# Kernel tuning notes

Measured on AMD Instinct MI355X. Metric: run time of the kernel, lower is better.

## Reference

```python
import jax, jax.numpy as jnp
import numpy as np

HID = 1024
HEADS = 16
HEAD_DIM = HID // HEADS


def setup_inputs() -> dict:
    key = jax.random.key(0)
    ks = jax.random.split(key, 11)
    s = 1.0 / np.sqrt(HID)
    return {
        "query": jax.random.normal(ks[0], (4, 2048, HID), jnp.float32),
        "key": jax.random.normal(ks[1], (4, 2048, HID), jnp.float32),
        "value": jax.random.normal(ks[2], (4, 2048, HID), jnp.float32),
        "wq": jax.random.normal(ks[3], (HID, HID), jnp.float32) * s,
        "bq": jnp.zeros((HID,), jnp.float32),
        "wk": jax.random.normal(ks[4], (HID, HID), jnp.float32) * s,
        "bk": jnp.zeros((HID,), jnp.float32),
        "wv": jax.random.normal(ks[5], (HID, HID), jnp.float32) * s,
        "bv": jnp.zeros((HID,), jnp.float32),
        "wo": jax.random.normal(ks[6], (HID, HID), jnp.float32) * s,
        "bo": jnp.zeros((HID,), jnp.float32),
    }


def reference(query, key, value, wq, bq, wk, bk, wv, bv, wo, bo):
    b, s, _ = query.shape
    scale = jnp.sqrt(jnp.asarray(HEAD_DIM, query.dtype))
    # linear projections; weights stored as [in, out]
    Q = (query @ wq + bq).reshape(b, s, HEADS, HEAD_DIM).transpose(0, 2, 1, 3)
    K = (key @ wk + bk).reshape(b, s, HEADS, HEAD_DIM).transpose(0, 2, 1, 3)
    V = (value @ wv + bv).reshape(b, s, HEADS, HEAD_DIM).transpose(0, 2, 1, 3)
    energy = jnp.einsum('bhqd,bhkd->bhqk', Q, K) / scale  # [B,H,S,S]
    attention = jax.nn.softmax(energy, axis=-1)  # dropout p=0 -> identity
    x = jnp.einsum('bhqk,bhkd->bhqd', attention, V)
    x = x.transpose(0, 2, 1, 3).reshape(b, s, HID)
    return x @ wo + bo
```

## Files before the change

kernel.cpp:

```cpp
#include <hip/hip_runtime.h>
#include <hip/hip_bf16.h>

#define B_   4
#define S_   2048
#define HID_ 1024
#define H_   16
#define D_   64
#define M_   (B_ * S_)

typedef __attribute__((ext_vector_type(8))) short bf16x8;
typedef __attribute__((ext_vector_type(4))) float f32x4;

#define GAS __attribute__((address_space(1)))
#define LAS __attribute__((address_space(3)))

__device__ __forceinline__ unsigned short f2bf(float f) {
    union { float f; unsigned int u; } x; x.f = f;
    unsigned int u = x.u;
    return (unsigned short)((u + 0x7fffu + ((u >> 16) & 1u)) >> 16);
}

__global__ __launch_bounds__(256)
void cast_bf16(const float* __restrict__ in, unsigned short* __restrict__ out) {
    const int i = blockIdx.x * 256 + threadIdx.x;
    const f32x4 a = ((const f32x4*)in)[i * 2];
    const f32x4 b = ((const f32x4*)in)[i * 2 + 1];
    bf16x8 v;
#pragma unroll
    for (int j = 0; j < 4; j++) { v[j] = (short)f2bf(a[j]); v[4 + j] = (short)f2bf(b[j]); }
    ((bf16x8*)out)[i] = v;
}

__global__ void transpose_cast(const float* __restrict__ w0, const float* __restrict__ w1,
                               const float* __restrict__ w2, const float* __restrict__ w3,
                               unsigned short* __restrict__ o0, unsigned short* __restrict__ o1,
                               unsigned short* __restrict__ o2, unsigned short* __restrict__ o3) {
    __shared__ float t[32][33];
    const float* w = (blockIdx.z == 0) ? w0 : (blockIdx.z == 1) ? w1 : (blockIdx.z == 2) ? w2 : w3;
    unsigned short* o = (blockIdx.z == 0) ? o0 : (blockIdx.z == 1) ? o1 : (blockIdx.z == 2) ? o2 : o3;
    const int tx = threadIdx.x, ty = threadIdx.y;
    const int bx = blockIdx.x * 32, by = blockIdx.y * 32;
#pragma unroll
    for (int i = 0; i < 4; i++)
        t[ty + i * 8][tx] = w[(size_t)(by + ty + i * 8) * HID_ + bx + tx];
    __syncthreads();
#pragma unroll
    for (int i = 0; i < 4; i++)
        o[(size_t)(bx + ty + i * 8) * HID_ + by + tx] = f2bf(t[tx][ty + i * 8]);
}

template <int MODE>
__global__ __launch_bounds__(256)
void gemm_k(const unsigned short* __restrict__ A, const unsigned short* __restrict__ Bt,
            const float* __restrict__ bias, void* __restrict__ outp, float oscale) {
    constexpr int BK = 32;
    __shared__ unsigned short As[128 * BK];
    __shared__ unsigned short Bs[128 * BK];

    const int tid  = threadIdx.x;
    const int lane = tid & 63;
    const int wave = tid >> 6;
    const int quad = lane >> 4;
    const int col  = lane & 15;
    const int wm   = (wave & 1) * 64;
    const int wn   = (wave >> 1) * 64;
    const int m0   = blockIdx.x * 128;
    const int n0   = blockIdx.y * 128;

    const int grow = wave * 16 + (lane >> 2);
    const int gcol = (lane & 3) * 8;
    const unsigned short* agp = A  + (size_t)(m0 + grow) * HID_ + gcol;
    const unsigned short* bgp = Bt + (size_t)(n0 + grow) * HID_ + gcol;
    unsigned short* asb = &As[wave * 512];
    unsigned short* bsb = &Bs[wave * 512];

    f32x4 zero; zero[0] = 0.f; zero[1] = 0.f; zero[2] = 0.f; zero[3] = 0.f;
    f32x4 acc[4][4];
#pragma unroll
    for (int mi = 0; mi < 4; mi++)
#pragma unroll
        for (int ni = 0; ni < 4; ni++) acc[mi][ni] = zero;

    for (int kt = 0; kt < HID_; kt += BK) {
        __builtin_amdgcn_global_load_lds((const GAS unsigned int*)(agp + kt),
                                         (LAS unsigned int*)asb, 16, 0, 0);
        __builtin_amdgcn_global_load_lds((const GAS unsigned int*)(agp + kt + (size_t)64 * HID_),
                                         (LAS unsigned int*)(asb + 2048), 16, 0, 0);
        __builtin_amdgcn_global_load_lds((const GAS unsigned int*)(bgp + kt),
                                         (LAS unsigned int*)bsb, 16, 0, 0);
        __builtin_amdgcn_global_load_lds((const GAS unsigned int*)(bgp + kt + (size_t)64 * HID_),
                                         (LAS unsigned int*)(bsb + 2048), 16, 0, 0);
        __syncthreads();

        bf16x8 af[4], bfr[4];
#pragma unroll
        for (int i = 0; i < 4; i++) af[i]  = *(const bf16x8*)&As[(wm + i * 16 + col) * BK + quad * 8];
#pragma unroll
        for (int i = 0; i < 4; i++) bfr[i] = *(const bf16x8*)&Bs[(wn + i * 16 + col) * BK + quad * 8];
#pragma unroll
        for (int mi = 0; mi < 4; mi++)
#pragma unroll
            for (int ni = 0; ni < 4; ni++)
                acc[mi][ni] = __builtin_amdgcn_mfma_f32_16x16x32_bf16(af[mi], bfr[ni], acc[mi][ni], 0, 0, 0);
        __syncthreads();
    }

#pragma unroll
    for (int ni = 0; ni < 4; ni++) {
        const int gn = n0 + wn + ni * 16 + col;
        const float bv = bias[gn];
#pragma unroll
        for (int mi = 0; mi < 4; mi++) {
#pragma unroll
            for (int i = 0; i < 4; i++) {
                const int gm = m0 + wm + mi * 16 + quad * 4 + i;
                const float v = (acc[mi][ni][i] + bv) * oscale;
                if constexpr (MODE == 2) {
                    ((float*)outp)[(size_t)gm * HID_ + gn] = v;
                } else if constexpr (MODE == 0) {
                    const int b = gm >> 11, s = gm & (S_ - 1), h = gn >> 6, d = gn & 63;
                    ((unsigned short*)outp)[(((size_t)b * H_ + h) * S_ + s) * D_ + d] = f2bf(v);
                } else {
                    const int b = gm >> 11, s = gm & (S_ - 1), h = gn >> 6, d = gn & 63;
                    ((unsigned short*)outp)[(((size_t)b * H_ + h) * D_ + d) * S_ + s] = f2bf(v);
                }
            }
        }
    }
}

__global__ __launch_bounds__(256)
void attn_k(const unsigned short* __restrict__ Qp, const unsigned short* __restrict__ Kp,
            const unsigned short* __restrict__ Vt, unsigned short* __restrict__ Xc) {
    constexpr int LK = 72;
    __shared__ unsigned short Ks[64 * LK];
    __shared__ unsigned short Vs[64 * LK];
    __shared__ unsigned short Pb[4][16 * LK];

    const int tid  = threadIdx.x;
    const int lane = tid & 63;
    const int wave = tid >> 6;
    const int quad = lane >> 4;
    const int col  = lane & 15;
    const int bh   = blockIdx.y;
    const int q0   = blockIdx.x * 64 + wave * 16;

    const unsigned short* Qb = Qp + (size_t)bh * S_ * D_;
    const unsigned short* Kb = Kp + (size_t)bh * S_ * D_;
    const unsigned short* Vb = Vt + (size_t)bh * D_ * S_;

    const bf16x8 qf0 = *(const bf16x8*)&Qb[(q0 + col) * D_ + quad * 8];
    const bf16x8 qf1 = *(const bf16x8*)&Qb[(q0 + col) * D_ + 32 + quad * 8];

    const int srow = tid >> 3;
    const int sseg = (tid & 7) * 8;

    f32x4 zero; zero[0] = 0.f; zero[1] = 0.f; zero[2] = 0.f; zero[3] = 0.f;
    f32x4 o[4];
#pragma unroll
    for (int t = 0; t < 4; t++) o[t] = zero;
    float lpart = 0.f;
    unsigned short* pb = &Pb[wave][0];

    for (int c0 = 0; c0 < S_; c0 += 64) {
        {
            const unsigned short* kg = Kb + (size_t)c0 * D_;
#pragma unroll
            for (int p = 0; p < 2; p++) {
                const int row = p * 32 + srow;
                *(bf16x8*)&Ks[row * LK + sseg] = *(const bf16x8*)&kg[row * D_ + sseg];
                *(bf16x8*)&Vs[row * LK + sseg] = *(const bf16x8*)&Vb[(size_t)row * S_ + c0 + sseg];
            }
        }
        __syncthreads();

        f32x4 e[4];
#pragma unroll
        for (int kt = 0; kt < 4; kt++) {
            const bf16x8 ka = *(const bf16x8*)&Ks[(kt * 16 + col) * LK + quad * 8];
            const bf16x8 kb = *(const bf16x8*)&Ks[(kt * 16 + col) * LK + 32 + quad * 8];
            e[kt] = __builtin_amdgcn_mfma_f32_16x16x32_bf16(ka, qf0, zero, 0, 0, 0);
            e[kt] = __builtin_amdgcn_mfma_f32_16x16x32_bf16(kb, qf1, e[kt], 0, 0, 0);
        }

#pragma unroll
        for (int kt = 0; kt < 4; kt++) {
            float p0 = __builtin_amdgcn_exp2f(e[kt][0]);
            float p1 = __builtin_amdgcn_exp2f(e[kt][1]);
            float p2 = __builtin_amdgcn_exp2f(e[kt][2]);
            float p3 = __builtin_amdgcn_exp2f(e[kt][3]);
            lpart += (p0 + p1) + (p2 + p3);
            const unsigned int u0 = __builtin_bit_cast(unsigned int, p0) + 0x8000u;
            const unsigned int u1 = __builtin_bit_cast(unsigned int, p1) + 0x8000u;
            const unsigned int u2 = __builtin_bit_cast(unsigned int, p2) + 0x8000u;
            const unsigned int u3 = __builtin_bit_cast(unsigned int, p3) + 0x8000u;
            uint2 w;
            w.x = __builtin_amdgcn_perm(u1, u0, 0x07060302u);
            w.y = __builtin_amdgcn_perm(u3, u2, 0x07060302u);
            *(uint2*)&pb[col * LK + kt * 16 + quad * 4] = w;
        }

#pragma unroll
        for (int ch = 0; ch < 2; ch++) {
            const bf16x8 pf = *(const bf16x8*)&pb[col * LK + ch * 32 + quad * 8];
#pragma unroll
            for (int t = 0; t < 4; t++) {
                const bf16x8 vf = *(const bf16x8*)&Vs[(t * 16 + col) * LK + ch * 32 + quad * 8];
                o[t] = __builtin_amdgcn_mfma_f32_16x16x32_bf16(vf, pf, o[t], 0, 0, 0);
            }
        }
        __syncthreads();
    }

    float l = lpart;
    l += __shfl_xor(l, 16);
    l += __shfl_xor(l, 32);
    const float inv = 1.f / l;

    const int b = bh >> 4, h = bh & 15;
    const int s = q0 + col;
    unsigned short* xp = &Xc[((size_t)(b * S_ + s)) * HID_ + h * D_];
#pragma unroll
    for (int t = 0; t < 4; t++) {
#pragma unroll
        for (int ii = 0; ii < 2; ii++) {
            const float v0 = o[t][ii * 2] * inv;
            const float v1 = o[t][ii * 2 + 1] * inv;
            const unsigned int wv_ = (unsigned int)f2bf(v0) | ((unsigned int)f2bf(v1) << 16);
            *(unsigned int*)&xp[t * 16 + quad * 4 + ii * 2] = wv_;
        }
    }
}

extern "C" void kernel_launch(void* const* d_in, const int* in_sizes, int n_in,
                              void* d_out, int out_size, void* d_ws, size_t ws_size,
                              hipStream_t stream) {
    (void)in_sizes; (void)n_in; (void)out_size; (void)ws_size;
    const float* query = (const float*)d_in[0];
    const float* key   = (const float*)d_in[1];
    const float* value = (const float*)d_in[2];
    const float* wq    = (const float*)d_in[3];
    const float* bq    = (const float*)d_in[4];
    const float* wk    = (const float*)d_in[5];
    const float* bk    = (const float*)d_in[6];
    const float* wv    = (const float*)d_in[7];
    const float* bv    = (const float*)d_in[8];
    const float* wo    = (const float*)d_in[9];
    const float* bo    = (const float*)d_in[10];
    float* out = (float*)d_out;

    unsigned short* ws  = (unsigned short*)d_ws;
    const size_t WSZ = (size_t)HID_ * HID_;
    const size_t TSZ = (size_t)M_ * HID_;
    unsigned short* wqT = ws;
    unsigned short* wkT = wqT + WSZ;
    unsigned short* wvT = wkT + WSZ;
    unsigned short* woT = wvT + WSZ;
    unsigned short* Qp  = woT + WSZ;
    unsigned short* Kp  = Qp + TSZ;
    unsigned short* Vt  = Kp + TSZ;
    unsigned short* Xc  = Vt + TSZ;
    unsigned short* Xb  = Xc + TSZ;

    const float cvt = 0.125f * 1.44269504f;

    transpose_cast<<<dim3(32, 32, 4), dim3(32, 8), 0, stream>>>(wq, wk, wv, wo, wqT, wkT, wvT, woT);

    const dim3 gg(M_ / 128, HID_ / 128);
    const int cg = (M_ * HID_ / 8) / 256;

    cast_bf16<<<cg, 256, 0, stream>>>(query, Xb);
    gemm_k<0><<<gg, 256, 0, stream>>>(Xb, wqT, bq, Qp, cvt);
    cast_bf16<<<cg, 256, 0, stream>>>(key, Xb);
    gemm_k<0><<<gg, 256, 0, stream>>>(Xb, wkT, bk, Kp, 1.f);
    cast_bf16<<<cg, 256, 0, stream>>>(value, Xb);
    gemm_k<1><<<gg, 256, 0, stream>>>(Xb, wvT, bv, Vt, 1.f);

    attn_k<<<dim3(S_ / 64, B_ * H_), 256, 0, stream>>>(Qp, Kp, Vt, Xc);

    gemm_k<2><<<gg, 256, 0, stream>>>(Xc, woT, bo, out, 1.f);
}
```

Measured before the change: 412.5 us.

## Use 32x32 MFMA in attention and stage GEMM epilogue through LDS

The attention kernel moves from 16x16x32 to 32x32x16 bf16 MFMA with 32 queries per wave and 128 queries per block, which halves the grid and increases reuse of each K/V tile loaded into LDS. The projection GEMM epilogues for Q/K and V now pack bf16 results into a shared buffer and write 16-byte vectorized stores to the head-major and transposed layouts, replacing scattered 2-byte stores. For MODE 0 the MFMA operand order is swapped so each lane holds contiguous output columns. This costs extra shared memory, extra barriers and higher register pressure from the f32x16 accumulators.

```diff
diff --git a/kernel.cpp b/kernel.cpp
--- a/kernel.cpp
+++ b/kernel.cpp
@@ -8,8 +8,9 @@
 #define D_   64
 #define M_   (B_ * S_)
 
-typedef __attribute__((ext_vector_type(8))) short bf16x8;
-typedef __attribute__((ext_vector_type(4))) float f32x4;
+typedef __attribute__((ext_vector_type(8)))  short bf16x8;
+typedef __attribute__((ext_vector_type(4)))  float f32x4;
+typedef __attribute__((ext_vector_type(16))) float f32x16;
 
 #define GAS __attribute__((address_space(1)))
 #define LAS __attribute__((address_space(3)))
@@ -54,8 +55,9 @@
 void gemm_k(const unsigned short* __restrict__ A, const unsigned short* __restrict__ Bt,
             const float* __restrict__ bias, void* __restrict__ outp, float oscale) {
     constexpr int BK = 32;
-    __shared__ unsigned short As[128 * BK];
-    __shared__ unsigned short Bs[128 * BK];
+    __shared__ unsigned short smem[8704];
+    unsigned short* As = smem;
+    unsigned short* Bs = smem + 4096;
 
     const int tid  = threadIdx.x;
     const int lane = tid & 63;
@@ -100,31 +102,80 @@
 #pragma unroll
         for (int mi = 0; mi < 4; mi++)
 #pragma unroll
-            for (int ni = 0; ni < 4; ni++)
-                acc[mi][ni] = __builtin_amdgcn_mfma_f32_16x16x32_bf16(af[mi], bfr[ni], acc[mi][ni], 0, 0, 0);
+            for (int ni = 0; ni < 4; ni++) {
+                if constexpr (MODE == 0)
+                    acc[mi][ni] = __builtin_amdgcn_mfma_f32_16x16x32_bf16(bfr[ni], af[mi], acc[mi][ni], 0, 0, 0);
+                else
+                    acc[mi][ni] = __builtin_amdgcn_mfma_f32_16x16x32_bf16(af[mi], bfr[ni], acc[mi][ni], 0, 0, 0);
+            }
         __syncthreads();
     }
 
-#pragma unroll
-    for (int ni = 0; ni < 4; ni++) {
-        const int gn = n0 + wn + ni * 16 + col;
-        const float bv = bias[gn];
-#pragma unroll
-        for (int mi = 0; mi < 4; mi++) {
-#pragma unroll
-            for (int i = 0; i < 4; i++) {
-                const int gm = m0 + wm + mi * 16 + quad * 4 + i;
-                const float v = (acc[mi][ni][i] + bv) * oscale;
-                if constexpr (MODE == 2) {
-                    ((float*)outp)[(size_t)gm * HID_ + gn] = v;
-                } else if constexpr (MODE == 0) {
-                    const int b = gm >> 11, s = gm & (S_ - 1), h = gn >> 6, d = gn & 63;
-                    ((unsigned short*)outp)[(((size_t)b * H_ + h) * S_ + s) * D_ + d] = f2bf(v);
+    if constexpr (MODE == 2) {
+#pragma unroll
+        for (int ni = 0; ni < 4; ni++) {
+            const int gn = n0 + wn + ni * 16 + col;
+            const float bv = bias[gn];
+#pragma unroll
+            for (int mi = 0; mi < 4; mi++)
+#pragma unroll
+                for (int i = 0; i < 4; i++) {
+                    const int gm = m0 + wm + mi * 16 + quad * 4 + i;
+                    ((float*)outp)[(size_t)gm * HID_ + gn] = acc[mi][ni][i] + bv;
+                }
+        }
+    } else {
+        unsigned short* RB = smem;
+#pragma unroll
+        for (int ph = 0; ph < 2; ph++) {
+            const bool writer = (MODE == 0) ? ((wave & 1) == ph) : ((wave >> 1) == ph);
+            if (writer) {
+#pragma unroll
+                for (int ni = 0; ni < 4; ni++) {
+                    if constexpr (MODE == 0) {
+                        const f32x4 bv = *(const f32x4*)&bias[n0 + wn + ni * 16 + quad * 4];
+#pragma unroll
+                        for (int mi = 0; mi < 4; mi++) {
+                            unsigned int u0 = f2bf((acc[mi][ni][0] + bv[0]) * oscale);
+                            unsigned int u1 = f2bf((acc[mi][ni][1] + bv[1]) * oscale);
+                            unsigned int u2 = f2bf((acc[mi][ni][2] + bv[2]) * oscale);
+                            unsigned int u3 = f2bf((acc[mi][ni][3] + bv[3]) * oscale);
+                            uint2 w; w.x = u0 | (u1 << 16); w.y = u2 | (u3 << 16);
+                            *(uint2*)&RB[(mi * 16 + col) * 136 + wn + ni * 16 + quad * 4] = w;
+                        }
+                    } else {
+                        const float bv = bias[n0 + wn + ni * 16 + col];
+#pragma unroll
+                        for (int mi = 0; mi < 4; mi++) {
+                            unsigned int u0 = f2bf(acc[mi][ni][0] + bv);
+                            unsigned int u1 = f2bf(acc[mi][ni][1] + bv);
+                            unsigned int u2 = f2bf(acc[mi][ni][2] + bv);
+                            unsigned int u3 = f2bf(acc[mi][ni][3] + bv);
+                            uint2 w; w.x = u0 | (u1 << 16); w.y = u2 | (u3 << 16);
+                            *(uint2*)&RB[(ni * 16 + col) * 136 + wm + mi * 16 + quad * 4] = w;
+                        }
+                    }
+                }
+            }
+            __syncthreads();
+#pragma unroll
+            for (int it = 0; it < 4; it++) {
+                const int c   = it * 256 + tid;
+                const int row = c >> 4, ch = c & 15;
+                const bf16x8 v = *(const bf16x8*)&RB[row * 136 + ch * 8];
+                if constexpr (MODE == 0) {
+                    const int m = m0 + ph * 64 + row;
+                    const int dg = n0 + ch * 8;
+                    const int h = dg >> 6, d = dg & 63;
+                    *(bf16x8*)&((unsigned short*)outp)[(((size_t)(m >> 11) * H_ + h) * S_ + (m & 2047)) * D_ + d] = v;
                 } else {
-                    const int b = gm >> 11, s = gm & (S_ - 1), h = gn >> 6, d = gn & 63;
-                    ((unsigned short*)outp)[(((size_t)b * H_ + h) * D_ + d) * S_ + s] = f2bf(v);
+                    const int dg = n0 + ph * 64 + row;
+                    const int h = dg >> 6, d = dg & 63;
+                    const int m = m0 + ch * 8;
+                    *(bf16x8*)&((unsigned short*)outp)[(((size_t)(m >> 11) * H_ + h) * D_ + d) * S_ + (m & 2047)] = v;
                 }
             }
+            __syncthreads();
         }
     }
 }
@@ -132,104 +183,104 @@
 __global__ __launch_bounds__(256)
 void attn_k(const unsigned short* __restrict__ Qp, const unsigned short* __restrict__ Kp,
             const unsigned short* __restrict__ Vt, unsigned short* __restrict__ Xc) {
-    constexpr int LK = 72;
-    __shared__ unsigned short Ks[64 * LK];
-    __shared__ unsigned short Vs[64 * LK];
-    __shared__ unsigned short Pb[4][16 * LK];
+    constexpr int LT = 72;
+    __shared__ unsigned short Ks[64 * LT];
+    __shared__ unsigned short Vs[64 * LT];
+    __shared__ unsigned short Pb[4 * 32 * LT];
 
     const int tid  = threadIdx.x;
     const int lane = tid & 63;
     const int wave = tid >> 6;
-    const int quad = lane >> 4;
-    const int col  = lane & 15;
+    const int l31  = lane & 31;
+    const int hw   = lane >> 5;
     const int bh   = blockIdx.y;
-    const int q0   = blockIdx.x * 64 + wave * 16;
+    const int q0   = blockIdx.x * 128 + wave * 32;
 
     const unsigned short* Qb = Qp + (size_t)bh * S_ * D_;
     const unsigned short* Kb = Kp + (size_t)bh * S_ * D_;
     const unsigned short* Vb = Vt + (size_t)bh * D_ * S_;
 
-    const bf16x8 qf0 = *(const bf16x8*)&Qb[(q0 + col) * D_ + quad * 8];
-    const bf16x8 qf1 = *(const bf16x8*)&Qb[(q0 + col) * D_ + 32 + quad * 8];
-
-    const int srow = tid >> 3;
-    const int sseg = (tid & 7) * 8;
-
-    f32x4 zero; zero[0] = 0.f; zero[1] = 0.f; zero[2] = 0.f; zero[3] = 0.f;
-    f32x4 o[4];
-#pragma unroll
-    for (int t = 0; t < 4; t++) o[t] = zero;
+    bf16x8 qf[4];
+#pragma unroll
+    for (int ks = 0; ks < 4; ks++)
+        qf[ks] = *(const bf16x8*)&Qb[(q0 + l31) * D_ + ks * 16 + hw * 8];
+
+    f32x16 o[2];
+#pragma unroll
+    for (int t = 0; t < 2; t++)
+#pragma unroll
+        for (int i = 0; i < 16; i++) o[t][i] = 0.f;
     float lpart = 0.f;
-    unsigned short* pb = &Pb[wave][0];
+    unsigned short* Pw = &Pb[wave * 32 * LT];
 
     for (int c0 = 0; c0 < S_; c0 += 64) {
-        {
-            const unsigned short* kg = Kb + (size_t)c0 * D_;
-#pragma unroll
-            for (int p = 0; p < 2; p++) {
-                const int row = p * 32 + srow;
-                *(bf16x8*)&Ks[row * LK + sseg] = *(const bf16x8*)&kg[row * D_ + sseg];
-                *(bf16x8*)&Vs[row * LK + sseg] = *(const bf16x8*)&Vb[(size_t)row * S_ + c0 + sseg];
-            }
+#pragma unroll
+        for (int it = 0; it < 2; it++) {
+            const int c = it * 256 + tid;
+            const int row = c >> 3, seg = (c & 7) * 8;
+            *(bf16x8*)&Ks[row * LT + seg] = *(const bf16x8*)&Kb[(size_t)(c0 + row) * D_ + seg];
+            *(bf16x8*)&Vs[row * LT + seg] = *(const bf16x8*)&Vb[(size_t)row * S_ + c0 + seg];
         }
         __syncthreads();
 
-        f32x4 e[4];
-#pragma unroll
-        for (int kt = 0; kt < 4; kt++) {
-            const bf16x8 ka = *(const bf16x8*)&Ks[(kt * 16 + col) * LK + quad * 8];
-            const bf16x8 kb = *(const bf16x8*)&Ks[(kt * 16 + col) * LK + 32 + quad * 8];
-            e[kt] = __builtin_amdgcn_mfma_f32_16x16x32_bf16(ka, qf0, zero, 0, 0, 0);
-            e[kt] = __builtin_amdgcn_mfma_f32_16x16x32_bf16(kb, qf1, e[kt], 0, 0, 0);
-        }
-
-#pragma unroll
-        for (int kt = 0; kt < 4; kt++) {
-            float p0 = __builtin_amdgcn_exp2f(e[kt][0]);
-            float p1 = __builtin_amdgcn_exp2f(e[kt][1]);
-            float p2 = __builtin_amdgcn_exp2f(e[kt][2]);
-            float p3 = __builtin_amdgcn_exp2f(e[kt][3]);
-            lpart += (p0 + p1) + (p2 + p3);
-            const unsigned int u0 = __builtin_bit_cast(unsigned int, p0) + 0x8000u;
-            const unsigned int u1 = __builtin_bit_cast(unsigned int, p1) + 0x8000u;
-            const unsigned int u2 = __builtin_bit_cast(unsigned int, p2) + 0x8000u;
-            const unsigned int u3 = __builtin_bit_cast(unsigned int, p3) + 0x8000u;
-            uint2 w;
-            w.x = __builtin_amdgcn_perm(u1, u0, 0x07060302u);
-            w.y = __builtin_amdgcn_perm(u3, u2, 0x07060302u);
-            *(uint2*)&pb[col * LK + kt * 16 + quad * 4] = w;
-        }
-
-#pragma unroll
-        for (int ch = 0; ch < 2; ch++) {
-            const bf16x8 pf = *(const bf16x8*)&pb[col * LK + ch * 32 + quad * 8];
-#pragma unroll
-            for (int t = 0; t < 4; t++) {
-                const bf16x8 vf = *(const bf16x8*)&Vs[(t * 16 + col) * LK + ch * 32 + quad * 8];
-                o[t] = __builtin_amdgcn_mfma_f32_16x16x32_bf16(vf, pf, o[t], 0, 0, 0);
+#pragma unroll
+        for (int g = 0; g < 2; g++) {
+            f32x16 e;
+#pragma unroll
+            for (int i = 0; i < 16; i++) e[i] = 0.f;
+#pragma unroll
+            for (int ks = 0; ks < 4; ks++) {
+                const bf16x8 a = *(const bf16x8*)&Ks[(g * 32 + l31) * LT + ks * 16 + hw * 8];
+                e = __builtin_amdgcn_mfma_f32_32x32x16_bf16(a, qf[ks], e, 0, 0, 0);
+            }
+#pragma unroll
+            for (int grp = 0; grp < 4; grp++) {
+                float p0 = __builtin_amdgcn_exp2f(e[grp * 4 + 0]);
+                float p1 = __builtin_amdgcn_exp2f(e[grp * 4 + 1]);
+                float p2 = __builtin_amdgcn_exp2f(e[grp * 4 + 2]);
+                float p3 = __builtin_amdgcn_exp2f(e[grp * 4 + 3]);
+                lpart += (p0 + p1) + (p2 + p3);
+                const unsigned int u0 = __builtin_bit_cast(unsigned int, p0) + 0x8000u;
+                const unsigned int u1 = __builtin_bit_cast(unsigned int, p1) + 0x8000u;
+                const unsigned int u2 = __builtin_bit_cast(unsigned int, p2) + 0x8000u;
+                const unsigned int u3 = __builtin_bit_cast(unsigned int, p3) + 0x8000u;
+                uint2 w;
+                w.x = __builtin_amdgcn_perm(u1, u0, 0x07060302u);
+                w.y = __builtin_amdgcn_perm(u3, u2, 0x07060302u);
+                *(uint2*)&Pw[l31 * LT + g * 32 + grp * 8 + hw * 4] = w;
+            }
+        }
+
+#pragma unroll
+        for (int ks = 0; ks < 4; ks++) {
+            const bf16x8 pf = *(const bf16x8*)&Pw[l31 * LT + ks * 16 + hw * 8];
+#pragma unroll
+            for (int t = 0; t < 2; t++) {
+                const bf16x8 vf = *(const bf16x8*)&Vs[(t * 32 + l31) * LT + ks * 16 + hw * 8];
+                o[t] = __builtin_amdgcn_mfma_f32_32x32x16_bf16(vf, pf, o[t], 0, 0, 0);
             }
         }
         __syncthreads();
     }
 
     float l = lpart;
-    l += __shfl_xor(l, 16);
     l += __shfl_xor(l, 32);
     const float inv = 1.f / l;
 
     const int b = bh >> 4, h = bh & 15;
-    const int s = q0 + col;
+    const int s = q0 + l31;
     unsigned short* xp = &Xc[((size_t)(b * S_ + s)) * HID_ + h * D_];
 #pragma unroll
-    for (int t = 0; t < 4; t++) {
-#pragma unroll
-        for (int ii = 0; ii < 2; ii++) {
-            const float v0 = o[t][ii * 2] * inv;
-            const float v1 = o[t][ii * 2 + 1] * inv;
-            const unsigned int wv_ = (unsigned int)f2bf(v0) | ((unsigned int)f2bf(v1) << 16);
-            *(unsigned int*)&xp[t * 16 + quad * 4 + ii * 2] = wv_;
-        }
-    }
+    for (int t = 0; t < 2; t++)
+#pragma unroll
+        for (int grp = 0; grp < 4; grp++) {
+            const unsigned int u0 = f2bf(o[t][grp * 4 + 0] * inv);
+            const unsigned int u1 = f2bf(o[t][grp * 4 + 1] * inv);
+            const unsigned int u2 = f2bf(o[t][grp * 4 + 2] * inv);
+            const unsigned int u3 = f2bf(o[t][grp * 4 + 3] * inv);
+            uint2 w; w.x = u0 | (u1 << 16); w.y = u2 | (u3 << 16);
+            *(uint2*)&xp[t * 32 + grp * 8 + hw * 4] = w;
+        }
 }
 
 extern "C" void kernel_launch(void* const* d_in, const int* in_sizes, int n_in,
@@ -276,7 +327,7 @@
     cast_bf16<<<cg, 256, 0, stream>>>(value, Xb);
     gemm_k<1><<<gg, 256, 0, stream>>>(Xb, wvT, bv, Vt, 1.f);
 
-    attn_k<<<dim3(S_ / 64, B_ * H_), 256, 0, stream>>>(Qp, Kp, Vt, Xc);
+    attn_k<<<dim3(S_ / 128, B_ * H_), 256, 0, stream>>>(Qp, Kp, Vt, Xc);
 
     gemm_k<2><<<gg, 256, 0, stream>>>(Xc, woT, bo, out, 1.f);
 }
```

Result: faster. 379.1 us (-8.1%).
